# Optimization experiments

Hardware: AMD Instinct MI355X
Metric: run time of the kernel (lower is better)

## Reference

```python
import jax, jax.numpy as jnp
import numpy as np
import math

N, D, H, E = 4096, 128, 8, 131072
HD = D // H  # head_dim = 16
SCALE = 1.0 / math.sqrt(HD)


def ln(x, g, b, eps=1e-5):
    m = x.mean(-1, keepdims=True)
    v = ((x - m) ** 2).mean(-1, keepdims=True)
    return (x - m) * jax.lax.rsqrt(v + eps) * g + b


def setup_inputs() -> dict:
    key = jax.random.key(0)
    ks = iter(jax.random.split(key, 40))

    def lin(out_d, in_d):
        w = jax.random.normal(next(ks), (out_d, in_d), jnp.float32) / math.sqrt(in_d)
        b = jnp.zeros((out_d,), jnp.float32)
        return w, b

    x = jax.random.normal(next(ks), (N, D), jnp.float32)
    edge_index = jax.random.randint(next(ks), (2, E), 0, N, dtype=jnp.int64)
    wq_l, bq_l = lin(D, D); wk_l, bk_l = lin(D, D); wv_l, bv_l = lin(D, D)
    wg, bg = lin(D, 2 * D)
    wq_g, bq_g = lin(D, D); wk_g, bk_g = lin(D, D); wv_g, bv_g = lin(D, D)
    wo_g, bo_g = lin(D, D)
    wf, bf = lin(D, 2 * D)
    gf = jnp.ones((D,), jnp.float32); betaf = jnp.zeros((D,), jnp.float32)
    w1, b1 = lin(4 * D, D); w2, b2 = lin(D, 4 * D)
    g1 = jnp.ones((D,), jnp.float32); be1 = jnp.zeros((D,), jnp.float32)
    g2 = jnp.ones((D,), jnp.float32); be2 = jnp.zeros((D,), jnp.float32)
    return dict(x=x, edge_index=edge_index,
                wq_l=wq_l, bq_l=bq_l, wk_l=wk_l, bk_l=bk_l, wv_l=wv_l, bv_l=bv_l,
                wg=wg, bg=bg,
                wq_g=wq_g, bq_g=bq_g, wk_g=wk_g, bk_g=bk_g, wv_g=wv_g, bv_g=bv_g,
                wo_g=wo_g, bo_g=bo_g,
                wf=wf, bf=bf, gf=gf, betaf=betaf,
                w1=w1, b1=b1, w2=w2, b2=b2,
                g1=g1, be1=be1, g2=g2, be2=be2)


def reference(x, edge_index, wq_l, bq_l, wk_l, bk_l, wv_l, bv_l, wg, bg,
              wq_g, bq_g, wk_g, bk_g, wv_g, bv_g, wo_g, bo_g,
              wf, bf, gf, betaf, w1, b1, w2, b2, g1, be1, g2, be2):
    src, dst = edge_index[0], edge_index[1]  # PyG: j=source, i=target
    # ---- local edge-indexed multi-head attention (GraphInteractionModule) ----
    Q = (x @ wq_l.T + bq_l).reshape(N, H, HD)
    K = (x @ wk_l.T + bk_l).reshape(N, H, HD)
    V = (x @ wv_l.T + bv_l).reshape(N, H, HD)
    attn = (Q[dst] * K[src]).sum(-1) * SCALE            # [E, H]
    m = jax.ops.segment_max(attn, dst, num_segments=N)  # [N, H]
    e = jnp.exp(attn - m[dst])
    s = jax.ops.segment_sum(e, dst, num_segments=N)
    alpha = e / s[dst]                                  # segment softmax over edges into each dst
    agg = jax.ops.segment_sum(V[src] * alpha[..., None], dst, num_segments=N).reshape(N, D)
    gate = jax.nn.sigmoid(jnp.concatenate([x, agg], axis=-1) @ wg.T + bg)
    local = gate * agg + (1.0 - gate) * x
    # ---- global dense MHA over all nodes (B=1) ----
    xn = ln(x, g1, be1)
    q = (xn @ wq_g.T + bq_g).reshape(N, H, HD)
    k = (xn @ wk_g.T + bk_g).reshape(N, H, HD)
    v = (xn @ wv_g.T + bv_g).reshape(N, H, HD)
    scores = jnp.einsum('nhd,mhd->hnm', q, k) * SCALE   # [H, N, N]
    p = jax.nn.softmax(scores, axis=-1)
    go = jnp.einsum('hnm,mhd->nhd', p, v).reshape(N, D) @ wo_g.T + bo_g
    # ---- fusion + residual + FFN ----
    fused = jax.nn.relu(ln(jnp.concatenate([local, go], axis=-1) @ wf.T + bf, gf, betaf))
    h = x + fused
    h2 = ln(h, g2, be2)
    out = h + (jax.nn.gelu(h2 @ w1.T + b1, approximate=False) @ w2.T + b2)
    return out
```

## Files before the change

### kernel.cpp

```cpp
#include <hip/hip_runtime.h>
#include <math.h>

#define NN 4096
#define DM 128
#define NE 131072
#define QSCALE 0.36067376022224085f
#define ESCALE 0.36067376022224085f

typedef short short8 __attribute__((ext_vector_type(8)));
typedef float f32x4  __attribute__((ext_vector_type(4)));
typedef unsigned int uint4v __attribute__((ext_vector_type(4)));

static __device__ __forceinline__ unsigned pk2(float lo, float hi) {
  union { float f; unsigned u; } a, b; a.f = lo; b.f = hi;
  return __builtin_amdgcn_perm(b.u + 0x8000u, a.u + 0x8000u, 0x07060302u);
}
static __device__ __forceinline__ unsigned pkp(float lo, float hi) {
  union { float f; unsigned u; } a, b; a.f = lo; b.f = hi;
  return __builtin_amdgcn_perm(b.u, a.u, 0x07060302u);
}
static __device__ __forceinline__ unsigned short f2bh(float f) {
  union { float f; unsigned u; } v; v.f = f;
  return (unsigned short)((v.u + 0x8000u) >> 16);
}
static __device__ __forceinline__ float b2f16(unsigned short u) {
  union { unsigned u; float f; } v; v.u = ((unsigned)u) << 16; return v.f;
}
static __device__ __forceinline__ short8 cvt8(float4 a, float4 b) {
  uint4v u;
  u.x = pk2(a.x, a.y); u.y = pk2(a.z, a.w);
  u.z = pk2(b.x, b.y); u.w = pk2(b.z, b.w);
  return __builtin_bit_cast(short8, u);
}
static __device__ __forceinline__ int detect64(const int* __restrict__ EI) {
  int v = EI[2 * (threadIdx.x & 63) + 1];
  for (int off = 1; off < 64; off <<= 1) v |= __shfl_xor(v, off);
  return (v == 0) ? 1 : 0;
}

__global__ __launch_bounds__(256) void k_fill(float* __restrict__ out, float v, int n) {
  int i = blockIdx.x * 256 + threadIdx.x;
  if (i < n) out[i] = v;
}

__global__ __launch_bounds__(256) void gemm_mfma(
    const float* __restrict__ A0, int lda0,
    const float* __restrict__ A1, int lda1, int ksplit,
    const float* __restrict__ Wt, const float* __restrict__ Bias,
    const float* __restrict__ Res, const float* __restrict__ E0, const float* __restrict__ E1,
    void* __restrict__ Cp, int Nt, int K, int act, int omode, float oscale)
{
  __shared__ short Asm[64][40];
  __shared__ short Wsm[64][40];
  const int m0 = blockIdx.x * 64, n0 = blockIdx.y * 64;
  const int tid = threadIdx.x;
  const int srow = tid >> 2, koff = (tid & 3) * 8;
  const int lane = tid & 63, wave = tid >> 6;
  const int quad = lane >> 4, m16 = lane & 15;
  f32x4 acc[4];
#pragma unroll
  for (int i = 0; i < 4; i++) acc[i] = {0.f, 0.f, 0.f, 0.f};

  for (int k0 = 0; k0 < K; k0 += 32) {
    const int kg = k0 + koff;
    const float* ap = (kg < ksplit) ? (A0 + (size_t)(m0 + srow) * lda0 + kg)
                                    : (A1 + (size_t)(m0 + srow) * lda1 + (kg - ksplit));
    float4 a0 = *(const float4*)ap, a1 = *(const float4*)(ap + 4);
    const float* wp = Wt + (size_t)(n0 + srow) * K + kg;
    float4 w0 = *(const float4*)wp, w1v = *(const float4*)(wp + 4);
    __syncthreads();
    *(short8*)&Asm[srow][koff] = cvt8(a0, a1);
    *(short8*)&Wsm[srow][koff] = cvt8(w0, w1v);
    __syncthreads();
    short8 af = *(short8*)&Asm[wave * 16 + m16][quad * 8];
#pragma unroll
    for (int nt = 0; nt < 4; nt++) {
      short8 bf = *(short8*)&Wsm[nt * 16 + m16][quad * 8];
      acc[nt] = __builtin_amdgcn_mfma_f32_16x16x32_bf16(af, bf, acc[nt], 0, 0, 0);
    }
  }
#pragma unroll
  for (int nt = 0; nt < 4; nt++) {
#pragma unroll
    for (int r = 0; r < 4; r++) {
      const int m = m0 + wave * 16 + quad * 4 + r;
      const int n = n0 + nt * 16 + m16;
      float v = acc[nt][r] + Bias[n];
      size_t oi = (size_t)m * Nt + n;
      if (act == 1) v = 0.5f * v * (1.0f + erff(v * 0.70710678118654752f));
      else if (act == 2) {
        float g = 1.0f / (1.0f + __expf(fminf(fmaxf(-v, -80.f), 80.f)));
        v = g * E0[oi] + (1.0f - g) * E1[oi];
      }
      if (Res) v += Res[oi];
      v *= oscale;
      if (omode == 0)      ((float*)Cp)[oi] = v;
      else if (omode == 1) ((unsigned short*)Cp)[oi] = f2bh(v);
      else                 ((unsigned short*)Cp)[(size_t)n * NN + m] = f2bh(v);
    }
  }
}

__global__ __launch_bounds__(256) void gemm_w2b(
    const unsigned short* __restrict__ A,
    const float* __restrict__ Wt, const float* __restrict__ Bias,
    const float* __restrict__ Res, float* __restrict__ Cp)
{
  __shared__ short Asm[64][40];
  __shared__ short Wsm[64][40];
  const int m0 = blockIdx.x * 64, n0 = blockIdx.y * 64;
  const int tid = threadIdx.x;
  const int srow = tid >> 2, koff = (tid & 3) * 8;
  const int lane = tid & 63, wave = tid >> 6;
  const int quad = lane >> 4, m16 = lane & 15;
  f32x4 acc[4];
#pragma unroll
  for (int i = 0; i < 4; i++) acc[i] = {0.f, 0.f, 0.f, 0.f};

  for (int k0 = 0; k0 < 512; k0 += 32) {
    const int kg = k0 + koff;
    short8 av = *(const short8*)(A + (size_t)(m0 + srow) * 512 + kg);
    const float* wp = Wt + (size_t)(n0 + srow) * 512 + kg;
    float4 w0 = *(const float4*)wp, w1v = *(const float4*)(wp + 4);
    __syncthreads();
    *(short8*)&Asm[srow][koff] = av;
    *(short8*)&Wsm[srow][koff] = cvt8(w0, w1v);
    __syncthreads();
    short8 af = *(short8*)&Asm[wave * 16 + m16][quad * 8];
#pragma unroll
    for (int nt = 0; nt < 4; nt++) {
      short8 bf = *(short8*)&Wsm[nt * 16 + m16][quad * 8];
      acc[nt] = __builtin_amdgcn_mfma_f32_16x16x32_bf16(af, bf, acc[nt], 0, 0, 0);
    }
  }
#pragma unroll
  for (int nt = 0; nt < 4; nt++) {
#pragma unroll
    for (int r = 0; r < 4; r++) {
      const int m = m0 + wave * 16 + quad * 4 + r;
      const int n = n0 + nt * 16 + m16;
      size_t oi = (size_t)m * 128 + n;
      Cp[oi] = acc[nt][r] + Bias[n] + Res[oi];
    }
  }
}

#define LN1(V, GV, BV) V = (V - mean) * rstd * GV + BV
__global__ __launch_bounds__(256) void gemm_six(
    const float* __restrict__ X,
    const float* __restrict__ G1, const float* __restrict__ Be1,
    const float* __restrict__ W0, const float* __restrict__ W1, const float* __restrict__ W2,
    const float* __restrict__ W3, const float* __restrict__ W4, const float* __restrict__ W5,
    const float* __restrict__ B0, const float* __restrict__ B1, const float* __restrict__ B2,
    const float* __restrict__ B3, const float* __restrict__ B4, const float* __restrict__ B5,
    void* __restrict__ O0, void* __restrict__ O1, void* __restrict__ O2,
    void* __restrict__ O3, void* __restrict__ O4, void* __restrict__ O5,
    int* __restrict__ deg)
{
  __shared__ short Asm[64][40];
  __shared__ short Wsm[64][40];
  if (blockIdx.x == 0 && blockIdx.y == 0) {
#pragma unroll
    for (int i = 0; i < 16; i++) deg[threadIdx.x * 16 + i] = 0;
  }
  const int g = blockIdx.y >> 1;
  const float* Wt  = (g==0)?W0:(g==1)?W1:(g==2)?W2:(g==3)?W3:(g==4)?W4:W5;
  const float* Bia = (g==0)?B0:(g==1)?B1:(g==2)?B2:(g==3)?B3:(g==4)?B4:B5;
  void* Cp         = (g==0)?O0:(g==1)?O1:(g==2)?O2:(g==3)?O3:(g==4)?O4:O5;
  const int omode  = (g==2)?1:(g==3)?1:(g==4)?3:(g==5)?2:0;
  const float osc  = (g==3)? QSCALE : (g==0)? ESCALE : 1.f;
  const int m0 = blockIdx.x * 64, n0 = (blockIdx.y & 1) * 64;
  const int tid = threadIdx.x;
  const int srow = tid >> 2, koff = (tid & 3) * 8;
  const int lane = tid & 63, wave = tid >> 6;
  const int quad = lane >> 4, m16 = lane & 15;

  const float* arow = X + (size_t)(m0 + srow) * 128 + koff;
  float4 a0[4], a1[4];
#pragma unroll
  for (int c = 0; c < 4; c++) {
    a0[c] = *(const float4*)(arow + c * 32);
    a1[c] = *(const float4*)(arow + c * 32 + 4);
  }
  if (g >= 3) {
    float s = 0.f;
#pragma unroll
    for (int c = 0; c < 4; c++)
      s += a0[c].x + a0[c].y + a0[c].z + a0[c].w + a1[c].x + a1[c].y + a1[c].z + a1[c].w;
    s += __shfl_xor(s, 1); s += __shfl_xor(s, 2);
    float mean = s * (1.0f / 128.0f);
    float v = 0.f;
#pragma unroll
    for (int c = 0; c < 4; c++) {
      float d;
      d = a0[c].x - mean; v += d*d;  d = a0[c].y - mean; v += d*d;
      d = a0[c].z - mean; v += d*d;  d = a0[c].w - mean; v += d*d;
      d = a1[c].x - mean; v += d*d;  d = a1[c].y - mean; v += d*d;
      d = a1[c].z - mean; v += d*d;  d = a1[c].w - mean; v += d*d;
    }
    v += __shfl_xor(v, 1); v += __shfl_xor(v, 2);
    float rstd = rsqrtf(v * (1.0f / 128.0f) + 1e-5f);
#pragma unroll
    for (int c = 0; c < 4; c++) {
      const int col = c * 32 + koff;
      float4 gv0 = *(const float4*)(G1 + col),  gv1 = *(const float4*)(G1 + col + 4);
      float4 bv0 = *(const float4*)(Be1 + col), bv1 = *(const float4*)(Be1 + col + 4);
      LN1(a0[c].x, gv0.x, bv0.x); LN1(a0[c].y, gv0.y, bv0.y);
      LN1(a0[c].z, gv0.z, bv0.z); LN1(a0[c].w, gv0.w, bv0.w);
      LN1(a1[c].x, gv1.x, bv1.x); LN1(a1[c].y, gv1.y, bv1.y);
      LN1(a1[c].z, gv1.z, bv1.z); LN1(a1[c].w, gv1.w, bv1.w);
    }
  }

  f32x4 acc[4];
#pragma unroll
  for (int i = 0; i < 4; i++) acc[i] = {0.f, 0.f, 0.f, 0.f};
#pragma unroll
  for (int c = 0; c < 4; c++) {
    const float* wp = Wt + (size_t)(n0 + srow) * 128 + c * 32 + koff;
    float4 w0 = *(const float4*)wp, w1v = *(const float4*)(wp + 4);
    __syncthreads();
    *(short8*)&Asm[srow][koff] = cvt8(a0[c], a1[c]);
    *(short8*)&Wsm[srow][koff] = cvt8(w0, w1v);
    __syncthreads();
    short8 af = *(short8*)&Asm[wave * 16 + m16][quad * 8];
#pragma unroll
    for (int nt = 0; nt < 4; nt++) {
      short8 bf = *(short8*)&Wsm[nt * 16 + m16][quad * 8];
      acc[nt] = __builtin_amdgcn_mfma_f32_16x16x32_bf16(af, bf, acc[nt], 0, 0, 0);
    }
  }
#pragma unroll
  for (int nt = 0; nt < 4; nt++) {
#pragma unroll
    for (int r = 0; r < 4; r++) {
      const int m = m0 + wave * 16 + quad * 4 + r;
      const int n = n0 + nt * 16 + m16;
      float v = (acc[nt][r] + Bia[n]) * osc;
      size_t oi = (size_t)m * 128 + n;
      if (omode == 0)      ((float*)Cp)[oi] = v;
      else if (omode == 1) ((unsigned short*)Cp)[oi] = f2bh(v);
      else if (omode == 3) ((unsigned short*)Cp)[(size_t)(n >> 4) * (NN * 16) + (size_t)m * 16 + (n & 15)] = f2bh(v);
      else                 ((unsigned short*)Cp)[(size_t)n * NN + m] = f2bh(v);
    }
  }
}

__global__ __launch_bounds__(256) void gemm_dual(
    const float* __restrict__ X, const float* __restrict__ AGG,
    const float* __restrict__ GO,
    const float* __restrict__ Wg, const float* __restrict__ Bg,
    const float* __restrict__ Wo, const float* __restrict__ Bo,
    float* __restrict__ LOCAL, float* __restrict__ GOP)
{
  __shared__ short Asm[64][40];
  __shared__ short Wsm[64][40];
  const int isGate = (blockIdx.y < 2);
  const float* A0  = isGate ? X   : GO;
  const float* A1  = isGate ? AGG : GO;
  const int ksplit = 128;
  const int K      = isGate ? 256 : 128;
  const float* Wt  = isGate ? Wg : Wo;
  const float* Bia = isGate ? Bg : Bo;
  float* Cp        = isGate ? LOCAL : GOP;
  const int m0 = blockIdx.x * 64, n0 = (blockIdx.y & 1) * 64;
  const int tid = threadIdx.x;
  const int srow = tid >> 2, koff = (tid & 3) * 8;
  const int lane = tid & 63, wave = tid >> 6;
  const int quad = lane >> 4, m16 = lane & 15;
  f32x4 acc[4];
#pragma unroll
  for (int i = 0; i < 4; i++) acc[i] = {0.f, 0.f, 0.f, 0.f};

  for (int k0 = 0; k0 < K; k0 += 32) {
    const int kg = k0 + koff;
    const float* ap = (kg < ksplit) ? (A0 + (size_t)(m0 + srow) * 128 + kg)
                                    : (A1 + (size_t)(m0 + srow) * 128 + (kg - ksplit));
    float4 a0 = *(const float4*)ap, a1 = *(const float4*)(ap + 4);
    const float* wp = Wt + (size_t)(n0 + srow) * K + kg;
    float4 w0 = *(const float4*)wp, w1v = *(const float4*)(wp + 4);
    __syncthreads();
    *(short8*)&Asm[srow][koff] = cvt8(a0, a1);
    *(short8*)&Wsm[srow][koff] = cvt8(w0, w1v);
    __syncthreads();
    short8 af = *(short8*)&Asm[wave * 16 + m16][quad * 8];
#pragma unroll
    for (int nt = 0; nt < 4; nt++) {
      short8 bf = *(short8*)&Wsm[nt * 16 + m16][quad * 8];
      acc[nt] = __builtin_amdgcn_mfma_f32_16x16x32_bf16(af, bf, acc[nt], 0, 0, 0);
    }
  }
#pragma unroll
  for (int nt = 0; nt < 4; nt++) {
#pragma unroll
    for (int r = 0; r < 4; r++) {
      const int m = m0 + wave * 16 + quad * 4 + r;
      const int n = n0 + nt * 16 + m16;
      float v = acc[nt][r] + Bia[n];
      size_t oi = (size_t)m * 128 + n;
      if (isGate) {
        float g = 1.0f / (1.0f + __expf(fminf(fmaxf(-v, -80.f), 80.f)));
        v = g * AGG[oi] + (1.0f - g) * X[oi];
      }
      Cp[oi] = v;
    }
  }
}

__global__ __launch_bounds__(512) void k_attn_fused(
    const unsigned short* __restrict__ Kh, const unsigned short* __restrict__ Qb,
    const unsigned short* __restrict__ VT, float* __restrict__ O,
    const int* __restrict__ EI, const float* __restrict__ Q, const float* __restrict__ Kl,
    unsigned short* __restrict__ EB, int* __restrict__ deg)
{
  __shared__ float LO[8][4][16][16];
  __shared__ float LL[8][4][16];
  if (blockIdx.x >= 512) {
    int is64 = detect64(EI);
    int gid = (blockIdx.x - 512) * 512 + threadIdx.x;
    int e = gid >> 3, hh = gid & 7;
    int s = is64 ? EI[2*e]      : EI[e];
    int d = is64 ? EI[2*(NE+e)] : EI[NE+e];
    s = min(max(s, 0), NN-1); d = min(max(d, 0), NN-1);
    const float4* qp = (const float4*)(Q  + (size_t)d * DM + hh * 16);
    const float4* kp = (const float4*)(Kl + (size_t)s * DM + hh * 16);
    float acc = 0.f;
#pragma unroll
    for (int c = 0; c < 4; c++) {
      float4 qa = qp[c], ka = kp[c];
      acc += qa.x*ka.x + qa.y*ka.y + qa.z*ka.z + qa.w*ka.w;
    }
    EB[(size_t)e*8 + hh] = f2bh(__builtin_amdgcn_exp2f(fminf(acc, 43.0f)));
    if (hh == 0) atomicAdd(&deg[d], 1);
    return;
  }
  const int h = blockIdx.x >> 6, qt = blockIdx.x & 63;
  const int tid = threadIdx.x, lane = tid & 63, wave = tid >> 6;
  const int quad = lane >> 4, m16 = lane & 15;
  const int r0 = qt * 64;
  const short8 z8 = {0,0,0,0,0,0,0,0};
  const f32x4  z4 = {0.f,0.f,0.f,0.f};
  short8 qf[4] = {z8, z8, z8, z8};
  if (quad < 2) {
#pragma unroll
    for (int j = 0; j < 4; j++)
      qf[j] = *(const short8*)(Qb + (size_t)(r0 + j * 16 + m16) * DM + h * 16 + quad * 8);
  }
  short8 ones;
#pragma unroll
  for (int i = 0; i < 8; i++) ones[i] = (short)0x3F80;
  const int kperm = (m16 >> 2) * 8 + (m16 & 3);
  const int kbase = wave * 512;
  const unsigned short* khead = Kh + (size_t)h * (NN * 16);
  f32x4 acc[4] = {z4, z4, z4, z4};
  f32x4 acc2[4] = {z4, z4, z4, z4};
  short8 a0 = z8, a1 = z8, a2 = z8, a3 = z8;
  for (int kt = 0; kt < 8; kt++) {
    const int key0 = kbase + kt * 64;
    if (quad < 2) {
      const unsigned short* kp = khead + (size_t)(key0 + kperm) * 16 + quad * 8;
      a0 = *(const short8*)kp;
      a1 = *(const short8*)(kp + 4 * 16);
      a2 = *(const short8*)(kp + 32 * 16);
      a3 = *(const short8*)(kp + 36 * 16);
    }
    const unsigned short* vp = VT + (size_t)(h * 16 + m16) * NN + key0 + quad * 8;
    short8 av0 = *(const short8*)vp;
    short8 av1 = *(const short8*)(vp + 32);
#pragma unroll
    for (int j = 0; j < 4; j++) {
      f32x4 s0 = __builtin_amdgcn_mfma_f32_16x16x32_bf16(a0, qf[j], z4, 0, 0, 0);
      f32x4 s1 = __builtin_amdgcn_mfma_f32_16x16x32_bf16(a1, qf[j], z4, 0, 0, 0);
      f32x4 s2 = __builtin_amdgcn_mfma_f32_16x16x32_bf16(a2, qf[j], z4, 0, 0, 0);
      f32x4 s3 = __builtin_amdgcn_mfma_f32_16x16x32_bf16(a3, qf[j], z4, 0, 0, 0);
      float e0 = __builtin_amdgcn_exp2f(s0[0]), e1 = __builtin_amdgcn_exp2f(s0[1]);
      float e2 = __builtin_amdgcn_exp2f(s0[2]), e3 = __builtin_amdgcn_exp2f(s0[3]);
      float e4 = __builtin_amdgcn_exp2f(s1[0]), e5 = __builtin_amdgcn_exp2f(s1[1]);
      float e6 = __builtin_amdgcn_exp2f(s1[2]), e7 = __builtin_amdgcn_exp2f(s1[3]);
      uint4v u;
      u.x = pkp(e0, e1); u.y = pkp(e2, e3); u.z = pkp(e4, e5); u.w = pkp(e6, e7);
      short8 p0 = __builtin_bit_cast(short8, u);
      float f0 = __builtin_amdgcn_exp2f(s2[0]), f1 = __builtin_amdgcn_exp2f(s2[1]);
      float f2 = __builtin_amdgcn_exp2f(s2[2]), f3 = __builtin_amdgcn_exp2f(s2[3]);
      float f4 = __builtin_amdgcn_exp2f(s3[0]), f5 = __builtin_amdgcn_exp2f(s3[1]);
      float f6 = __builtin_amdgcn_exp2f(s3[2]), f7 = __builtin_amdgcn_exp2f(s3[3]);
      uint4v w;
      w.x = pkp(f0, f1); w.y = pkp(f2, f3); w.z = pkp(f4, f5); w.w = pkp(f6, f7);
      short8 p1 = __builtin_bit_cast(short8, w);
      acc[j]  = __builtin_amdgcn_mfma_f32_16x16x32_bf16(av0, p0, acc[j], 0, 0, 0);
      acc[j]  = __builtin_amdgcn_mfma_f32_16x16x32_bf16(av1, p1, acc[j], 0, 0, 0);
      acc2[j] = __builtin_amdgcn_mfma_f32_16x16x32_bf16(ones, p0, acc2[j], 0, 0, 0);
      acc2[j] = __builtin_amdgcn_mfma_f32_16x16x32_bf16(ones, p1, acc2[j], 0, 0, 0);
    }
  }
#pragma unroll
  for (int j = 0; j < 4; j++) {
    float4 a4; a4.x = acc[j][0]; a4.y = acc[j][1]; a4.z = acc[j][2]; a4.w = acc[j][3];
    *(float4*)&LO[wave][j][m16][quad * 4] = a4;
    if (lane < 16) LL[wave][j][lane] = acc2[j][0];
  }
  __syncthreads();
  if (wave < 4) {
    const int j = wave;
    float4 o = *(float4*)&LO[0][j][m16][quad * 4];
    float lt = LL[0][j][m16];
#pragma unroll
    for (int w2 = 1; w2 < 8; w2++) {
      float4 t = *(float4*)&LO[w2][j][m16][quad * 4];
      o.x += t.x; o.y += t.y; o.z += t.z; o.w += t.w;
      lt += LL[w2][j][m16];
    }
    float inv = 1.0f / fmaxf(lt, 1e-30f);
    float4 r4; r4.x = o.x * inv; r4.y = o.y * inv; r4.z = o.z * inv; r4.w = o.w * inv;
    *(float4*)(O + (size_t)(r0 + j * 16 + m16) * DM + h * 16 + quad * 4) = r4;
  }
}

__global__ __launch_bounds__(256) void gemm_ffn1(
    const float* __restrict__ T, const float* __restrict__ X,
    const float* __restrict__ Gf, const float* __restrict__ Bef,
    const float* __restrict__ G2, const float* __restrict__ Be2,
    const float* __restrict__ W1, const float* __restrict__ B1,
    float* __restrict__ H, unsigned short* __restrict__ T1)
{
  __shared__ short Asm[64][40];
  __shared__ short Wsm[64][40];
  const int m0 = blockIdx.x * 64, n0 = blockIdx.y * 64;
  const int tid = threadIdx.x;
  const int srow = tid >> 2, koff = (tid & 3) * 8;
  const int lane = tid & 63, wave = tid >> 6;
  const int quad = lane >> 4, m16 = lane & 15;

  const float* trow = T + (size_t)(m0 + srow) * 128 + koff;
  const float* xrow = X + (size_t)(m0 + srow) * 128 + koff;
  float4 a0[4], a1[4];
#pragma unroll
  for (int c = 0; c < 4; c++) {
    a0[c] = *(const float4*)(trow + c * 32);
    a1[c] = *(const float4*)(trow + c * 32 + 4);
  }
  {
    float s = 0.f;
#pragma unroll
    for (int c = 0; c < 4; c++)
      s += a0[c].x + a0[c].y + a0[c].z + a0[c].w + a1[c].x + a1[c].y + a1[c].z + a1[c].w;
    s += __shfl_xor(s, 1); s += __shfl_xor(s, 2);
    float mean = s * (1.0f / 128.0f);
    float v = 0.f;
#pragma unroll
    for (int c = 0; c < 4; c++) {
      float d;
      d = a0[c].x - mean; v += d*d;  d = a0[c].y - mean; v += d*d;
      d = a0[c].z - mean; v += d*d;  d = a0[c].w - mean; v += d*d;
      d = a1[c].x - mean; v += d*d;  d = a1[c].y - mean; v += d*d;
      d = a1[c].z - mean; v += d*d;  d = a1[c].w - mean; v += d*d;
    }
    v += __shfl_xor(v, 1); v += __shfl_xor(v, 2);
    float rstd = rsqrtf(v * (1.0f / 128.0f) + 1e-5f);
#pragma unroll
    for (int c = 0; c < 4; c++) {
      const int col = c * 32 + koff;
      float4 gv0 = *(const float4*)(Gf + col),  gv1 = *(const float4*)(Gf + col + 4);
      float4 bv0 = *(const float4*)(Bef + col), bv1 = *(const float4*)(Bef + col + 4);
      float4 x0 = *(const float4*)(xrow + c * 32), x1 = *(const float4*)(xrow + c * 32 + 4);
      LN1(a0[c].x, gv0.x, bv0.x); LN1(a0[c].y, gv0.y, bv0.y);
      LN1(a0[c].z, gv0.z, bv0.z); LN1(a0[c].w, gv0.w, bv0.w);
      LN1(a1[c].x, gv1.x, bv1.x); LN1(a1[c].y, gv1.y, bv1.y);
      LN1(a1[c].z, gv1.z, bv1.z); LN1(a1[c].w, gv1.w, bv1.w);
      a0[c].x = x0.x + fmaxf(a0[c].x, 0.f); a0[c].y = x0.y + fmaxf(a0[c].y, 0.f);
      a0[c].z = x0.z + fmaxf(a0[c].z, 0.f); a0[c].w = x0.w + fmaxf(a0[c].w, 0.f);
      a1[c].x = x1.x + fmaxf(a1[c].x, 0.f); a1[c].y = x1.y + fmaxf(a1[c].y, 0.f);
      a1[c].z = x1.z + fmaxf(a1[c].z, 0.f); a1[c].w = x1.w + fmaxf(a1[c].w, 0.f);
      if (blockIdx.y == 0) {
        *(float4*)(H + (size_t)(m0 + srow) * 128 + c * 32 + koff)     = a0[c];
        *(float4*)(H + (size_t)(m0 + srow) * 128 + c * 32 + koff + 4) = a1[c];
      }
    }
  }
  {
    float s = 0.f;
#pragma unroll
    for (int c = 0; c < 4; c++)
      s += a0[c].x + a0[c].y + a0[c].z + a0[c].w + a1[c].x + a1[c].y + a1[c].z + a1[c].w;
    s += __shfl_xor(s, 1); s += __shfl_xor(s, 2);
    float mean = s * (1.0f / 128.0f);
    float v = 0.f;
#pragma unroll
    for (int c = 0; c < 4; c++) {
      float d;
      d = a0[c].x - mean; v += d*d;  d = a0[c].y - mean; v += d*d;
      d = a0[c].z - mean; v += d*d;  d = a0[c].w - mean; v += d*d;
      d = a1[c].x - mean; v += d*d;  d = a1[c].y - mean; v += d*d;
      d = a1[c].z - mean; v += d*d;  d = a1[c].w - mean; v += d*d;
    }
    v += __shfl_xor(v, 1); v += __shfl_xor(v, 2);
    float rstd = rsqrtf(v * (1.0f / 128.0f) + 1e-5f);
#pragma unroll
    for (int c = 0; c < 4; c++) {
      const int col = c * 32 + koff;
      float4 gv0 = *(const float4*)(G2 + col),  gv1 = *(const float4*)(G2 + col + 4);
      float4 bv0 = *(const float4*)(Be2 + col), bv1 = *(const float4*)(Be2 + col + 4);
      LN1(a0[c].x, gv0.x, bv0.x); LN1(a0[c].y, gv0.y, bv0.y);
      LN1(a0[c].z, gv0.z, bv0.z); LN1(a0[c].w, gv0.w, bv0.w);
      LN1(a1[c].x, gv1.x, bv1.x); LN1(a1[c].y, gv1.y, bv1.y);
      LN1(a1[c].z, gv1.z, bv1.z); LN1(a1[c].w, gv1.w, bv1.w);
    }
  }

  f32x4 acc[4];
#pragma unroll
  for (int i = 0; i < 4; i++) acc[i] = {0.f, 0.f, 0.f, 0.f};
#pragma unroll
  for (int c = 0; c < 4; c++) {
    const float* wp = W1 + (size_t)(n0 + srow) * 128 + c * 32 + koff;
    float4 w0 = *(const float4*)wp, w1v = *(const float4*)(wp + 4);
    __syncthreads();
    *(short8*)&Asm[srow][koff] = cvt8(a0[c], a1[c]);
    *(short8*)&Wsm[srow][koff] = cvt8(w0, w1v);
    __syncthreads();
    short8 af = *(short8*)&Asm[wave * 16 + m16][quad * 8];
#pragma unroll
    for (int nt = 0; nt < 4; nt++) {
      short8 bf = *(short8*)&Wsm[nt * 16 + m16][quad * 8];
      acc[nt] = __builtin_amdgcn_mfma_f32_16x16x32_bf16(af, bf, acc[nt], 0, 0, 0);
    }
  }
#pragma unroll
  for (int nt = 0; nt < 4; nt++) {
#pragma unroll
    for (int r = 0; r < 4; r++) {
      const int m = m0 + wave * 16 + quad * 4 + r;
      const int n = n0 + nt * 16 + m16;
      float v = acc[nt][r] + B1[n];
      v = 0.5f * v * (1.0f + erff(v * 0.70710678118654752f));
      T1[(size_t)m * 512 + n] = f2bh(v);
    }
  }
}

__global__ __launch_bounds__(256) void k_scan(const int* __restrict__ deg,
    int* __restrict__ offs, int* __restrict__ cursor) {
  __shared__ int sums[256];
  int t = threadIdx.x;
  int loc[16];
  int s = 0;
#pragma unroll
  for (int i = 0; i < 16; i++) { loc[i] = s; s += deg[t*16 + i]; }
  sums[t] = s;
  __syncthreads();
  for (int d = 1; d < 256; d <<= 1) {
    int v = (t >= d) ? sums[t - d] : 0;
    __syncthreads();
    sums[t] += v;
    __syncthreads();
  }
  int base = sums[t] - s;
#pragma unroll
  for (int i = 0; i < 16; i++) {
    offs[t*16 + i] = base + loc[i];
    cursor[t*16 + i] = base + loc[i];
  }
}
__global__ __launch_bounds__(256) void k_scatter(const int* __restrict__ EI,
    int* __restrict__ cursor, int* __restrict__ elist) {
  int is64 = detect64(EI);
  int e = blockIdx.x * 256 + threadIdx.x;
  int d = is64 ? EI[2*(NE+e)] : EI[NE+e];
  d = min(max(d, 0), NN-1);
  int slot = atomicAdd(&cursor[d], 1);
  elist[slot] = e;
}

__global__ __launch_bounds__(256) void k_edge_agg3(const int* __restrict__ EI,
    const int* __restrict__ deg, const int* __restrict__ offs,
    const int* __restrict__ elist, const unsigned short* __restrict__ Vl,
    const unsigned short* __restrict__ EB, float* __restrict__ AG) {
  __shared__ float PS[2][128];
  __shared__ float SSH[2][2][8];
  int is64 = detect64(EI);
  int tid = threadIdx.x;
  int dsti = tid >> 7;
  int half = (tid >> 6) & 1;
  int lane = tid & 63;
  int d = blockIdx.x * 2 + dsti;
  int degd = deg[d], start = offs[d];
  int hh = lane >> 3;
  float ss = 0.f;
  for (int i = (lane & 7) * 2 + half; i < degd; i += 16)
    ss += b2f16(EB[(size_t)elist[start + i] * 8 + hh]);
  for (int o = 1; o < 8; o <<= 1) ss += __shfl_xor(ss, o);
  if ((lane & 7) == 0) SSH[dsti][half][hh] = ss;
  __syncthreads();
  float inv = 1.0f / fmaxf(SSH[dsti][0][hh] + SSH[dsti][1][hh], 1e-30f);
  float ax = 0.f, ay = 0.f;
  int i = half;
  for (; i + 6 < degd; i += 8) {
    int e0 = elist[start+i], e1 = elist[start+i+2], e2 = elist[start+i+4], e3 = elist[start+i+6];
    int s0 = is64 ? EI[2*e0] : EI[e0];
    int s1 = is64 ? EI[2*e1] : EI[e1];
    int s2 = is64 ? EI[2*e2] : EI[e2];
    int s3 = is64 ? EI[2*e3] : EI[e3];
    s0 = min(max(s0,0),NN-1); s1 = min(max(s1,0),NN-1);
    s2 = min(max(s2,0),NN-1); s3 = min(max(s3,0),NN-1);
    float w0 = b2f16(EB[(size_t)e0*8 + hh]) * inv;
    float w1 = b2f16(EB[(size_t)e1*8 + hh]) * inv;
    float w2 = b2f16(EB[(size_t)e2*8 + hh]) * inv;
    float w3 = b2f16(EB[(size_t)e3*8 + hh]) * inv;
    unsigned v0 = *(const unsigned*)(Vl + (size_t)s0 * DM + 2 * lane);
    unsigned v1 = *(const unsigned*)(Vl + (size_t)s1 * DM + 2 * lane);
    unsigned v2 = *(const unsigned*)(Vl + (size_t)s2 * DM + 2 * lane);
    unsigned v3 = *(const unsigned*)(Vl + (size_t)s3 * DM + 2 * lane);
    ax += w0 * b2f16((unsigned short)(v0 & 0xffffu)) + w1 * b2f16((unsigned short)(v1 & 0xffffu))
        + w2 * b2f16((unsigned short)(v2 & 0xffffu)) + w3 * b2f16((unsigned short)(v3 & 0xffffu));
    ay += w0 * b2f16((unsigned short)(v0 >> 16)) + w1 * b2f16((unsigned short)(v1 >> 16))
        + w2 * b2f16((unsigned short)(v2 >> 16)) + w3 * b2f16((unsigned short)(v3 >> 16));
  }
  for (; i < degd; i += 2) {
    int e = elist[start + i];
    int s = is64 ? EI[2*e] : EI[e];
    s = min(max(s, 0), NN-1);
    float a = b2f16(EB[(size_t)e*8 + hh]) * inv;
    unsigned v = *(const unsigned*)(Vl + (size_t)s * DM + 2 * lane);
    ax += a * b2f16((unsigned short)(v & 0xffffu));
    ay += a * b2f16((unsigned short)(v >> 16));
  }
  if (half == 1) { PS[dsti][2*lane] = ax; PS[dsti][2*lane+1] = ay; }
  __syncthreads();
  if (half == 0) {
    float2 r; r.x = ax + PS[dsti][2*lane]; r.y = ay + PS[dsti][2*lane+1];
    *(float2*)(AG + (size_t)d * DM + 2 * lane) = r;
  }
}

extern "C" void kernel_launch(void* const* d_in, const int* in_sizes, int n_in,
                              void* d_out, int out_size, void* d_ws, size_t ws_size,
                              hipStream_t stream) {
  const float* x     = (const float*)d_in[0];
  const int*   ei    = (const int*)  d_in[1];
  const float* wq_l  = (const float*)d_in[2];  const float* bq_l = (const float*)d_in[3];
  const float* wk_l  = (const float*)d_in[4];  const float* bk_l = (const float*)d_in[5];
  const float* wv_l  = (const float*)d_in[6];  const float* bv_l = (const float*)d_in[7];
  const float* wg    = (const float*)d_in[8];  const float* bg   = (const float*)d_in[9];
  const float* wq_g  = (const float*)d_in[10]; const float* bq_g = (const float*)d_in[11];
  const float* wk_g  = (const float*)d_in[12]; const float* bk_g = (const float*)d_in[13];
  const float* wv_g  = (const float*)d_in[14]; const float* bv_g = (const float*)d_in[15];
  const float* wo_g  = (const float*)d_in[16]; const float* bo_g = (const float*)d_in[17];
  const float* wf    = (const float*)d_in[18]; const float* bff  = (const float*)d_in[19];
  const float* gf    = (const float*)d_in[20]; const float* betaf= (const float*)d_in[21];
  const float* w1    = (const float*)d_in[22]; const float* b1   = (const float*)d_in[23];
  const float* w2    = (const float*)d_in[24]; const float* b2   = (const float*)d_in[25];
  const float* g1    = (const float*)d_in[26]; const float* be1  = (const float*)d_in[27];
  const float* g2    = (const float*)d_in[28]; const float* be2  = (const float*)d_in[29];
  float* out = (float*)d_out;

  const size_t NEED = (size_t)3289088 * 4;
  if (ws_size < NEED) {
    k_fill<<<2048, 256, 0, stream>>>(out, 100.0f, NN*DM);
    return;
  }

  float* W = (float*)d_ws;
  float*          lQ    = W + 0;
  float*          lK    = W + 524288;
  unsigned short* lV    = (unsigned short*)(W + 1048576);
  unsigned short* eb    = (unsigned short*)(W + 1310720);
  float*          go    = W + 1835008;
  unsigned short* qgb   = (unsigned short*)(W + 2359296);
  unsigned short* kgb   = (unsigned short*)(W + 2621440);
  unsigned short* vgT   = (unsigned short*)(W + 2883584);
  float*          agg   = W + 0;
  float*          local_= W + 524288;
  float*          gop   = W + 1048576;
  float*          tmpf  = W + 2097152;
  float*          h     = W + 2621440;
  unsigned short* t1    = (unsigned short*)(W + 0);
  int* deg    = (int*)(W + 3145728);
  int* cursor = (int*)(W + 3149824);
  int* offs   = (int*)(W + 3153920);
  int* elist  = (int*)(W + 3158016);

  dim3 b256(256);

  gemm_six<<<dim3(64,12), b256, 0, stream>>>(x, g1, be1,
      wq_l, wk_l, wv_l, wq_g, wk_g, wv_g,
      bq_l, bk_l, bv_l, bq_g, bk_g, bv_g,
      lQ, lK, lV, qgb, kgb, vgT, deg);

  k_attn_fused<<<2560, dim3(512), 0, stream>>>(kgb, qgb, vgT, go, ei, lQ, lK, eb, deg);

  k_scan<<<1, b256, 0, stream>>>(deg, offs, cursor);
  k_scatter<<<512, b256, 0, stream>>>(ei, cursor, elist);
  k_edge_agg3<<<2048, b256, 0, stream>>>(ei, deg, offs, elist, lV, eb, agg);

  gemm_dual<<<dim3(64,4), b256, 0, stream>>>(x, agg, go, wg, bg, wo_g, bo_g, local_, gop);

  gemm_mfma<<<dim3(64,2), b256, 0, stream>>>(local_,128, gop,128,128, wf, bff,
      nullptr,nullptr,nullptr, tmpf, 128, 256, 0, 0, 1.f);

  gemm_ffn1<<<dim3(64,8), b256, 0, stream>>>(tmpf, x, gf, betaf, g2, be2, w1, b1, h, t1);
  gemm_w2b<<<dim3(64,2), b256, 0, stream>>>(t1, w2, b2, h, out);
}
```

Measured before the change: 221.0 us.

## Fold output projection into fusion weights and store local Q/K in bf16

Precomputes Wf[:,128:]·Wo_g and the matching folded bias inside extra blocks of the first GEMM launch. This removes the separate go→gop projection GEMM, and the fusion GEMM then consumes go directly with the combined weight. Local Q and K are also written as bf16 instead of fp32, which halves the gather traffic in the edge-score computation. In exchange it adds bf16 rounding to the edge attention logits and uses a small serial weight-product in otherwise idle blocks.

```diff
diff --git a/kernel.cpp b/kernel.cpp
--- a/kernel.cpp
+++ b/kernel.cpp
@@ -26,6 +26,12 @@
 static __device__ __forceinline__ float b2f16(unsigned short u) {
   union { unsigned u; float f; } v; v.u = ((unsigned)u) << 16; return v.f;
 }
+static __device__ __forceinline__ float blo(unsigned u) {
+  union { unsigned u; float f; } v; v.u = u << 16; return v.f;
+}
+static __device__ __forceinline__ float bhi(unsigned u) {
+  union { unsigned u; float f; } v; v.u = u & 0xffff0000u; return v.f;
+}
 static __device__ __forceinline__ short8 cvt8(float4 a, float4 b) {
   uint4v u;
   u.x = pk2(a.x, a.y); u.y = pk2(a.z, a.w);
@@ -41,108 +47,6 @@
 __global__ __launch_bounds__(256) void k_fill(float* __restrict__ out, float v, int n) {
   int i = blockIdx.x * 256 + threadIdx.x;
   if (i < n) out[i] = v;
-}
-
-__global__ __launch_bounds__(256) void gemm_mfma(
-    const float* __restrict__ A0, int lda0,
-    const float* __restrict__ A1, int lda1, int ksplit,
-    const float* __restrict__ Wt, const float* __restrict__ Bias,
-    const float* __restrict__ Res, const float* __restrict__ E0, const float* __restrict__ E1,
-    void* __restrict__ Cp, int Nt, int K, int act, int omode, float oscale)
-{
-  __shared__ short Asm[64][40];
-  __shared__ short Wsm[64][40];
-  const int m0 = blockIdx.x * 64, n0 = blockIdx.y * 64;
-  const int tid = threadIdx.x;
-  const int srow = tid >> 2, koff = (tid & 3) * 8;
-  const int lane = tid & 63, wave = tid >> 6;
-  const int quad = lane >> 4, m16 = lane & 15;
-  f32x4 acc[4];
-#pragma unroll
-  for (int i = 0; i < 4; i++) acc[i] = {0.f, 0.f, 0.f, 0.f};
-
-  for (int k0 = 0; k0 < K; k0 += 32) {
-    const int kg = k0 + koff;
-    const float* ap = (kg < ksplit) ? (A0 + (size_t)(m0 + srow) * lda0 + kg)
-                                    : (A1 + (size_t)(m0 + srow) * lda1 + (kg - ksplit));
-    float4 a0 = *(const float4*)ap, a1 = *(const float4*)(ap + 4);
-    const float* wp = Wt + (size_t)(n0 + srow) * K + kg;
-    float4 w0 = *(const float4*)wp, w1v = *(const float4*)(wp + 4);
-    __syncthreads();
-    *(short8*)&Asm[srow][koff] = cvt8(a0, a1);
-    *(short8*)&Wsm[srow][koff] = cvt8(w0, w1v);
-    __syncthreads();
-    short8 af = *(short8*)&Asm[wave * 16 + m16][quad * 8];
-#pragma unroll
-    for (int nt = 0; nt < 4; nt++) {
-      short8 bf = *(short8*)&Wsm[nt * 16 + m16][quad * 8];
-      acc[nt] = __builtin_amdgcn_mfma_f32_16x16x32_bf16(af, bf, acc[nt], 0, 0, 0);
-    }
-  }
-#pragma unroll
-  for (int nt = 0; nt < 4; nt++) {
-#pragma unroll
-    for (int r = 0; r < 4; r++) {
-      const int m = m0 + wave * 16 + quad * 4 + r;
-      const int n = n0 + nt * 16 + m16;
-      float v = acc[nt][r] + Bias[n];
-      size_t oi = (size_t)m * Nt + n;
-      if (act == 1) v = 0.5f * v * (1.0f + erff(v * 0.70710678118654752f));
-      else if (act == 2) {
-        float g = 1.0f / (1.0f + __expf(fminf(fmaxf(-v, -80.f), 80.f)));
-        v = g * E0[oi] + (1.0f - g) * E1[oi];
-      }
-      if (Res) v += Res[oi];
-      v *= oscale;
-      if (omode == 0)      ((float*)Cp)[oi] = v;
-      else if (omode == 1) ((unsigned short*)Cp)[oi] = f2bh(v);
-      else                 ((unsigned short*)Cp)[(size_t)n * NN + m] = f2bh(v);
-    }
-  }
-}
-
-__global__ __launch_bounds__(256) void gemm_w2b(
-    const unsigned short* __restrict__ A,
-    const float* __restrict__ Wt, const float* __restrict__ Bias,
-    const float* __restrict__ Res, float* __restrict__ Cp)
-{
-  __shared__ short Asm[64][40];
-  __shared__ short Wsm[64][40];
-  const int m0 = blockIdx.x * 64, n0 = blockIdx.y * 64;
-  const int tid = threadIdx.x;
-  const int srow = tid >> 2, koff = (tid & 3) * 8;
-  const int lane = tid & 63, wave = tid >> 6;
-  const int quad = lane >> 4, m16 = lane & 15;
-  f32x4 acc[4];
-#pragma unroll
-  for (int i = 0; i < 4; i++) acc[i] = {0.f, 0.f, 0.f, 0.f};
-
-  for (int k0 = 0; k0 < 512; k0 += 32) {
-    const int kg = k0 + koff;
-    short8 av = *(const short8*)(A + (size_t)(m0 + srow) * 512 + kg);
-    const float* wp = Wt + (size_t)(n0 + srow) * 512 + kg;
-    float4 w0 = *(const float4*)wp, w1v = *(const float4*)(wp + 4);
-    __syncthreads();
-    *(short8*)&Asm[srow][koff] = av;
-    *(short8*)&Wsm[srow][koff] = cvt8(w0, w1v);
-    __syncthreads();
-    short8 af = *(short8*)&Asm[wave * 16 + m16][quad * 8];
-#pragma unroll
-    for (int nt = 0; nt < 4; nt++) {
-      short8 bf = *(short8*)&Wsm[nt * 16 + m16][quad * 8];
-      acc[nt] = __builtin_amdgcn_mfma_f32_16x16x32_bf16(af, bf, acc[nt], 0, 0, 0);
-    }
-  }
-#pragma unroll
-  for (int nt = 0; nt < 4; nt++) {
-#pragma unroll
-    for (int r = 0; r < 4; r++) {
-      const int m = m0 + wave * 16 + quad * 4 + r;
-      const int n = n0 + nt * 16 + m16;
-      size_t oi = (size_t)m * 128 + n;
-      Cp[oi] = acc[nt][r] + Bias[n] + Res[oi];
-    }
-  }
 }
 
 #define LN1(V, GV, BV) V = (V - mean) * rstd * GV + BV
@@ -155,10 +59,37 @@
     const float* __restrict__ B3, const float* __restrict__ B4, const float* __restrict__ B5,
     void* __restrict__ O0, void* __restrict__ O1, void* __restrict__ O2,
     void* __restrict__ O3, void* __restrict__ O4, void* __restrict__ O5,
-    int* __restrict__ deg)
+    int* __restrict__ deg,
+    const float* __restrict__ WFp, const float* __restrict__ WOg, const float* __restrict__ BOg,
+    float* __restrict__ WCp, float* __restrict__ BFp)
 {
   __shared__ short Asm[64][40];
   __shared__ short Wsm[64][40];
+  if (blockIdx.y == 12) {
+    if (blockIdx.x >= 16) return;
+    const int c = threadIdx.x & 127;
+    const int f0 = blockIdx.x * 8 + (threadIdx.x >> 7) * 4;
+    const float* wf0 = WFp + (size_t)(f0 + 0) * 256 + 128;
+    const float* wf1 = WFp + (size_t)(f0 + 1) * 256 + 128;
+    const float* wf2 = WFp + (size_t)(f0 + 2) * 256 + 128;
+    const float* wf3 = WFp + (size_t)(f0 + 3) * 256 + 128;
+    float a0v = 0.f, a1v = 0.f, a2v = 0.f, a3v = 0.f;
+    float c0 = 0.f, c1 = 0.f, c2 = 0.f, c3 = 0.f;
+#pragma unroll 4
+    for (int n = 0; n < 128; n++) {
+      float wo = WOg[(size_t)n * 128 + c];
+      float bv = BOg[n];
+      float w0 = wf0[n], w1 = wf1[n], w2 = wf2[n], w3 = wf3[n];
+      a0v += w0 * wo; a1v += w1 * wo; a2v += w2 * wo; a3v += w3 * wo;
+      c0 += w0 * bv; c1 += w1 * bv; c2 += w2 * bv; c3 += w3 * bv;
+    }
+    WCp[(size_t)(f0 + 0) * 128 + c] = a0v;
+    WCp[(size_t)(f0 + 1) * 128 + c] = a1v;
+    WCp[(size_t)(f0 + 2) * 128 + c] = a2v;
+    WCp[(size_t)(f0 + 3) * 128 + c] = a3v;
+    if (c == 0) { BFp[f0] = c0; BFp[f0 + 1] = c1; BFp[f0 + 2] = c2; BFp[f0 + 3] = c3; }
+    return;
+  }
   if (blockIdx.x == 0 && blockIdx.y == 0) {
 #pragma unroll
     for (int i = 0; i < 16; i++) deg[threadIdx.x * 16 + i] = 0;
@@ -167,7 +98,7 @@
   const float* Wt  = (g==0)?W0:(g==1)?W1:(g==2)?W2:(g==3)?W3:(g==4)?W4:W5;
   const float* Bia = (g==0)?B0:(g==1)?B1:(g==2)?B2:(g==3)?B3:(g==4)?B4:B5;
   void* Cp         = (g==0)?O0:(g==1)?O1:(g==2)?O2:(g==3)?O3:(g==4)?O4:O5;
-  const int omode  = (g==2)?1:(g==3)?1:(g==4)?3:(g==5)?2:0;
+  const int omode  = (g==4)?3:(g==5)?2:1;
   const float osc  = (g==3)? QSCALE : (g==0)? ESCALE : 1.f;
   const int m0 = blockIdx.x * 64, n0 = (blockIdx.y & 1) * 64;
   const int tid = threadIdx.x;
@@ -238,32 +169,21 @@
       const int n = n0 + nt * 16 + m16;
       float v = (acc[nt][r] + Bia[n]) * osc;
       size_t oi = (size_t)m * 128 + n;
-      if (omode == 0)      ((float*)Cp)[oi] = v;
-      else if (omode == 1) ((unsigned short*)Cp)[oi] = f2bh(v);
+      if (omode == 1)      ((unsigned short*)Cp)[oi] = f2bh(v);
       else if (omode == 3) ((unsigned short*)Cp)[(size_t)(n >> 4) * (NN * 16) + (size_t)m * 16 + (n & 15)] = f2bh(v);
       else                 ((unsigned short*)Cp)[(size_t)n * NN + m] = f2bh(v);
     }
   }
 }
 
-__global__ __launch_bounds__(256) void gemm_dual(
+__global__ __launch_bounds__(256) void gemm_gate(
     const float* __restrict__ X, const float* __restrict__ AGG,
-    const float* __restrict__ GO,
     const float* __restrict__ Wg, const float* __restrict__ Bg,
-    const float* __restrict__ Wo, const float* __restrict__ Bo,
-    float* __restrict__ LOCAL, float* __restrict__ GOP)
+    float* __restrict__ LOCAL)
 {
   __shared__ short Asm[64][40];
   __shared__ short Wsm[64][40];
-  const int isGate = (blockIdx.y < 2);
-  const float* A0  = isGate ? X   : GO;
-  const float* A1  = isGate ? AGG : GO;
-  const int ksplit = 128;
-  const int K      = isGate ? 256 : 128;
-  const float* Wt  = isGate ? Wg : Wo;
-  const float* Bia = isGate ? Bg : Bo;
-  float* Cp        = isGate ? LOCAL : GOP;
-  const int m0 = blockIdx.x * 64, n0 = (blockIdx.y & 1) * 64;
+  const int m0 = blockIdx.x * 64, n0 = blockIdx.y * 64;
   const int tid = threadIdx.x;
   const int srow = tid >> 2, koff = (tid & 3) * 8;
   const int lane = tid & 63, wave = tid >> 6;
@@ -272,12 +192,12 @@
 #pragma unroll
   for (int i = 0; i < 4; i++) acc[i] = {0.f, 0.f, 0.f, 0.f};
 
-  for (int k0 = 0; k0 < K; k0 += 32) {
+  for (int k0 = 0; k0 < 256; k0 += 32) {
     const int kg = k0 + koff;
-    const float* ap = (kg < ksplit) ? (A0 + (size_t)(m0 + srow) * 128 + kg)
-                                    : (A1 + (size_t)(m0 + srow) * 128 + (kg - ksplit));
+    const float* ap = (kg < 128) ? (X + (size_t)(m0 + srow) * 128 + kg)
+                                 : (AGG + (size_t)(m0 + srow) * 128 + (kg - 128));
     float4 a0 = *(const float4*)ap, a1 = *(const float4*)(ap + 4);
-    const float* wp = Wt + (size_t)(n0 + srow) * K + kg;
+    const float* wp = Wg + (size_t)(n0 + srow) * 256 + kg;
     float4 w0 = *(const float4*)wp, w1v = *(const float4*)(wp + 4);
     __syncthreads();
     *(short8*)&Asm[srow][koff] = cvt8(a0, a1);
@@ -296,13 +216,58 @@
     for (int r = 0; r < 4; r++) {
       const int m = m0 + wave * 16 + quad * 4 + r;
       const int n = n0 + nt * 16 + m16;
-      float v = acc[nt][r] + Bia[n];
+      float v = acc[nt][r] + Bg[n];
       size_t oi = (size_t)m * 128 + n;
-      if (isGate) {
-        float g = 1.0f / (1.0f + __expf(fminf(fmaxf(-v, -80.f), 80.f)));
-        v = g * AGG[oi] + (1.0f - g) * X[oi];
-      }
-      Cp[oi] = v;
+      float gg = 1.0f / (1.0f + __expf(fminf(fmaxf(-v, -80.f), 80.f)));
+      LOCAL[oi] = gg * AGG[oi] + (1.0f - gg) * X[oi];
+    }
+  }
+}
+
+__global__ __launch_bounds__(256) void gemm_fuse(
+    const float* __restrict__ LOCAL, const float* __restrict__ GO,
+    const float* __restrict__ WF, const float* __restrict__ WC,
+    const float* __restrict__ BF, const float* __restrict__ BFOLD,
+    float* __restrict__ OUT)
+{
+  __shared__ short Asm[64][40];
+  __shared__ short Wsm[64][40];
+  const int m0 = blockIdx.x * 64, n0 = blockIdx.y * 64;
+  const int tid = threadIdx.x;
+  const int srow = tid >> 2, koff = (tid & 3) * 8;
+  const int lane = tid & 63, wave = tid >> 6;
+  const int quad = lane >> 4, m16 = lane & 15;
+  f32x4 acc[4];
+#pragma unroll
+  for (int i = 0; i < 4; i++) acc[i] = {0.f, 0.f, 0.f, 0.f};
+
+  for (int k0 = 0; k0 < 256; k0 += 32) {
+    const int kg = k0 + koff;
+    const float* ap = (kg < 128) ? (LOCAL + (size_t)(m0 + srow) * 128 + kg)
+                                 : (GO + (size_t)(m0 + srow) * 128 + (kg - 128));
+    float4 a0 = *(const float4*)ap, a1 = *(const float4*)(ap + 4);
+    const float* wp = (kg < 128) ? (WF + (size_t)(n0 + srow) * 256 + kg)
+                                 : (WC + (size_t)(n0 + srow) * 128 + (kg - 128));
+    float4 w0 = *(const float4*)wp, w1v = *(const float4*)(wp + 4);
+    __syncthreads();
+    *(short8*)&Asm[srow][koff] = cvt8(a0, a1);
+    *(short8*)&Wsm[srow][koff] = cvt8(w0, w1v);
+    __syncthreads();
+    short8 af = *(short8*)&Asm[wave * 16 + m16][quad * 8];
+#pragma unroll
+    for (int nt = 0; nt < 4; nt++) {
+      short8 bf = *(short8*)&Wsm[nt * 16 + m16][quad * 8];
+      acc[nt] = __builtin_amdgcn_mfma_f32_16x16x32_bf16(af, bf, acc[nt], 0, 0, 0);
+    }
+  }
+#pragma unroll
+  for (int nt = 0; nt < 4; nt++) {
+#pragma unroll
+    for (int r = 0; r < 4; r++) {
+      const int m = m0 + wave * 16 + quad * 4 + r;
+      const int n = n0 + nt * 16 + m16;
+      size_t oi = (size_t)m * 128 + n;
+      OUT[oi] = acc[nt][r] + BF[n] + BFOLD[n];
     }
   }
 }
@@ -310,7 +275,8 @@
 __global__ __launch_bounds__(512) void k_attn_fused(
     const unsigned short* __restrict__ Kh, const unsigned short* __restrict__ Qb,
     const unsigned short* __restrict__ VT, float* __restrict__ O,
-    const int* __restrict__ EI, const float* __restrict__ Q, const float* __restrict__ Kl,
+    const int* __restrict__ EI, const unsigned short* __restrict__ Qb16,
+    const unsigned short* __restrict__ Kb16,
     unsigned short* __restrict__ EB, int* __restrict__ deg)
 {
   __shared__ float LO[8][4][16][16];
@@ -322,13 +288,15 @@
     int s = is64 ? EI[2*e]      : EI[e];
     int d = is64 ? EI[2*(NE+e)] : EI[NE+e];
     s = min(max(s, 0), NN-1); d = min(max(d, 0), NN-1);
-    const float4* qp = (const float4*)(Q  + (size_t)d * DM + hh * 16);
-    const float4* kp = (const float4*)(Kl + (size_t)s * DM + hh * 16);
+    const uint4v* qp = (const uint4v*)(Qb16 + (size_t)d * DM + hh * 16);
+    const uint4v* kp = (const uint4v*)(Kb16 + (size_t)s * DM + hh * 16);
+    uint4v qa = qp[0], qb2 = qp[1];
+    uint4v ka = kp[0], kb2 = kp[1];
     float acc = 0.f;
 #pragma unroll
-    for (int c = 0; c < 4; c++) {
-      float4 qa = qp[c], ka = kp[c];
-      acc += qa.x*ka.x + qa.y*ka.y + qa.z*ka.z + qa.w*ka.w;
+    for (int i2 = 0; i2 < 4; i2++) {
+      acc += blo(qa[i2]) * blo(ka[i2]) + bhi(qa[i2]) * bhi(ka[i2]);
+      acc += blo(qb2[i2]) * blo(kb2[i2]) + bhi(qb2[i2]) * bhi(kb2[i2]);
     }
     EB[(size_t)e*8 + hh] = f2bh(__builtin_amdgcn_exp2f(fminf(acc, 43.0f)));
     if (hh == 0) atomicAdd(&deg[d], 1);
@@ -534,6 +502,50 @@
       float v = acc[nt][r] + B1[n];
       v = 0.5f * v * (1.0f + erff(v * 0.70710678118654752f));
       T1[(size_t)m * 512 + n] = f2bh(v);
+    }
+  }
+}
+
+__global__ __launch_bounds__(256) void gemm_w2b(
+    const unsigned short* __restrict__ A,
+    const float* __restrict__ Wt, const float* __restrict__ Bias,
+    const float* __restrict__ Res, float* __restrict__ Cp)
+{
+  __shared__ short Asm[64][40];
+  __shared__ short Wsm[64][40];
+  const int m0 = blockIdx.x * 64, n0 = blockIdx.y * 64;
+  const int tid = threadIdx.x;
+  const int srow = tid >> 2, koff = (tid & 3) * 8;
+  const int lane = tid & 63, wave = tid >> 6;
+  const int quad = lane >> 4, m16 = lane & 15;
+  f32x4 acc[4];
+#pragma unroll
+  for (int i = 0; i < 4; i++) acc[i] = {0.f, 0.f, 0.f, 0.f};
+
+  for (int k0 = 0; k0 < 512; k0 += 32) {
+    const int kg = k0 + koff;
+    short8 av = *(const short8*)(A + (size_t)(m0 + srow) * 512 + kg);
+    const float* wp = Wt + (size_t)(n0 + srow) * 512 + kg;
+    float4 w0 = *(const float4*)wp, w1v = *(const float4*)(wp + 4);
+    __syncthreads();
+    *(short8*)&Asm[srow][koff] = av;
+    *(short8*)&Wsm[srow][koff] = cvt8(w0, w1v);
+    __syncthreads();
+    short8 af = *(short8*)&Asm[wave * 16 + m16][quad * 8];
+#pragma unroll
+    for (int nt = 0; nt < 4; nt++) {
+      short8 bf = *(short8*)&Wsm[nt * 16 + m16][quad * 8];
+      acc[nt] = __builtin_amdgcn_mfma_f32_16x16x32_bf16(af, bf, acc[nt], 0, 0, 0);
+    }
+  }
+#pragma unroll
+  for (int nt = 0; nt < 4; nt++) {
+#pragma unroll
+    for (int r = 0; r < 4; r++) {
+      const int m = m0 + wave * 16 + quad * 4 + r;
+      const int n = n0 + nt * 16 + m16;
+      size_t oi = (size_t)m * 128 + n;
+      Cp[oi] = acc[nt][r] + Bias[n] + Res[oi];
     }
   }
 }
@@ -653,15 +665,15 @@
   const float* g2    = (const float*)d_in[28]; const float* be2  = (const float*)d_in[29];
   float* out = (float*)d_out;
 
-  const size_t NEED = (size_t)3289088 * 4;
+  const size_t NEED = (size_t)3305600 * 4;
   if (ws_size < NEED) {
     k_fill<<<2048, 256, 0, stream>>>(out, 100.0f, NN*DM);
     return;
   }
 
   float* W = (float*)d_ws;
-  float*          lQ    = W + 0;
-  float*          lK    = W + 524288;
+  unsigned short* lQb   = (unsigned short*)(W + 0);
+  unsigned short* lKb   = (unsigned short*)(W + 524288);
   unsigned short* lV    = (unsigned short*)(W + 1048576);
   unsigned short* eb    = (unsigned short*)(W + 1310720);
   float*          go    = W + 1835008;
@@ -670,7 +682,6 @@
   unsigned short* vgT   = (unsigned short*)(W + 2883584);
   float*          agg   = W + 0;
   float*          local_= W + 524288;
-  float*          gop   = W + 1048576;
   float*          tmpf  = W + 2097152;
   float*          h     = W + 2621440;
   unsigned short* t1    = (unsigned short*)(W + 0);
@@ -678,24 +689,26 @@
   int* cursor = (int*)(W + 3149824);
   int* offs   = (int*)(W + 3153920);
   int* elist  = (int*)(W + 3158016);
+  float* Wc    = W + 3289088;
+  float* bfold = W + 3305472;
 
   dim3 b256(256);
 
-  gemm_six<<<dim3(64,12), b256, 0, stream>>>(x, g1, be1,
+  gemm_six<<<dim3(64,13), b256, 0, stream>>>(x, g1, be1,
       wq_l, wk_l, wv_l, wq_g, wk_g, wv_g,
       bq_l, bk_l, bv_l, bq_g, bk_g, bv_g,
-      lQ, lK, lV, qgb, kgb, vgT, deg);
-
-  k_attn_fused<<<2560, dim3(512), 0, stream>>>(kgb, qgb, vgT, go, ei, lQ, lK, eb, deg);
+      lQb, lKb, lV, qgb, kgb, vgT, deg,
+      wf, wo_g, bo_g, Wc, bfold);
+
+  k_attn_fused<<<2560, dim3(512), 0, stream>>>(kgb, qgb, vgT, go, ei, lQb, lKb, eb, deg);
 
   k_scan<<<1, b256, 0, stream>>>(deg, offs, cursor);
   k_scatter<<<512, b256, 0, stream>>>(ei, cursor, elist);
   k_edge_agg3<<<2048, b256, 0, stream>>>(ei, deg, offs, elist, lV, eb, agg);
 
-  gemm_dual<<<dim3(64,4), b256, 0, stream>>>(x, agg, go, wg, bg, wo_g, bo_g, local_, gop);
-
-  gemm_mfma<<<dim3(64,2), b256, 0, stream>>>(local_,128, gop,128,128, wf, bff,
-      nullptr,nullptr,nullptr, tmpf, 128, 256, 0, 0, 1.f);
+  gemm_gate<<<dim3(64,2), b256, 0, stream>>>(x, agg, wg, bg, local_);
+
+  gemm_fuse<<<dim3(64,2), b256, 0, stream>>>(local_, go, wf, Wc, bff, bfold, tmpf);
 
   gemm_ffn1<<<dim3(64,8), b256, 0, stream>>>(tmpf, x, gf, betaf, g2, be2, w1, b1, h, t1);
   gemm_w2b<<<dim3(64,2), b256, 0, stream>>>(t1, w2, b2, h, out);
```

After: 220.2 us. Within noise of the previous version (-0.4%).
